# Performance work log

Measured on AMD Instinct MI355X. Metric: run time of the kernel, lower is better.

## Reference

```python
import jax, jax.numpy as jnp
import numpy as np

BN_EPS = 1e-5

# Octonion multiplication table: hamilton block (r, c) = SIGN[c][r] * a[IDX[c][r]]
IDX = np.array([
    [0,1,2,3,4,5,6,7],
    [1,0,3,2,5,4,7,6],
    [2,3,0,1,6,7,4,5],
    [3,2,1,0,7,6,5,4],
    [4,5,6,7,0,1,2,3],
    [5,4,7,6,1,0,3,2],
    [6,7,4,5,2,3,0,1],
    [7,6,5,4,3,2,1,0]], dtype=np.int32)
SIGN = np.array([
    [ 1, 1, 1, 1, 1, 1, 1, 1],
    [ 1,-1, 1,-1, 1,-1,-1, 1],
    [ 1,-1,-1, 1, 1, 1,-1,-1],
    [ 1, 1,-1,-1, 1,-1, 1,-1],
    [ 1,-1,-1,-1,-1, 1, 1, 1],
    [ 1, 1,-1, 1,-1,-1,-1, 1],
    [ 1, 1, 1,-1,-1, 1,-1,-1],
    [ 1,-1, 1, 1,-1,-1, 1,-1]], dtype=np.float32)

def make_octonion_mul(kernel):
    # kernel: [in/8, out]; split cols into 8 chunks a0..a7 of [in/8, out/8]
    in8, out = kernel.shape
    out8 = out // 8
    a = kernel.reshape(in8, 8, out8).transpose(1, 0, 2)  # [8, in/8, out/8]
    blocks = jnp.asarray(SIGN)[:, :, None, None] * a[jnp.asarray(IDX)]  # [c, r, in/8, out/8]
    # hamilton[r*in8:(r+1)*in8, c*out8:(c+1)*out8] = blocks[c, r]
    return jnp.transpose(blocks, (1, 2, 0, 3)).reshape(8 * in8, out)  # [in, out]

def setup_inputs() -> dict:
    key = jax.random.key(0)
    ks = jax.random.split(key, 5)
    N, E, D_IN, D_OUT = 100000, 3200000, 256, 256
    stdv = float(np.sqrt(6.0 / (D_IN // 8 + D_OUT)))
    return {
        "x": jax.random.normal(ks[0], (N, D_IN), dtype=jnp.float32),
        "weight": jax.random.uniform(ks[1], (D_IN // 8, D_OUT), dtype=jnp.float32,
                                      minval=-stdv, maxval=stdv),
        "gamma": jnp.ones((D_OUT,), dtype=jnp.float32),
        "beta": jnp.zeros((D_OUT,), dtype=jnp.float32),
        "edge_weight": jax.random.uniform(ks[2], (E,), dtype=jnp.float32),
        "edge_src": jax.random.randint(ks[3], (E,), 0, N, dtype=jnp.int32),
        "edge_dst": jax.random.randint(ks[4], (E,), 0, N, dtype=jnp.int32),
    }

def reference(x, weight, gamma, beta, edge_weight, edge_src, edge_dst):
    N = x.shape[0]
    hamilton = make_octonion_mul(weight)          # [in, out]
    support = x @ hamilton                        # [N, out]
    # sparse adjacency aggregation: out[dst] += w * support[src]
    msgs = edge_weight[:, None] * support[edge_src]
    out = jax.ops.segment_sum(msgs, edge_dst, num_segments=N)  # [N, out]
    # BatchNorm1d (training mode: batch stats, biased variance)
    mean = jnp.mean(out, axis=0)
    var = jnp.var(out, axis=0)
    out = (out - mean) * jax.lax.rsqrt(var + BN_EPS) * gamma + beta
    return jnp.tanh(out)
```

## Files before the change

kernel.cpp:

```cpp
#include <hip/hip_runtime.h>
#include <cmath>

#define NB 1024
#define CHUNK 16384

typedef short short8 __attribute__((ext_vector_type(8)));
typedef float f32x4 __attribute__((ext_vector_type(4)));

__constant__ int c_IDX[64] = {
  0,1,2,3,4,5,6,7,
  1,0,3,2,5,4,7,6,
  2,3,0,1,6,7,4,5,
  3,2,1,0,7,6,5,4,
  4,5,6,7,0,1,2,3,
  5,4,7,6,1,0,3,2,
  6,7,4,5,2,3,0,1,
  7,6,5,4,3,2,1,0};
__constant__ float c_SIGN[64] = {
  1,1,1,1,1,1,1,1,
  1,-1,1,-1,1,-1,-1,1,
  1,-1,-1,1,1,1,-1,-1,
  1,1,-1,-1,1,-1,1,-1,
  1,-1,-1,-1,-1,1,1,1,
  1,1,-1,1,-1,-1,-1,1,
  1,1,1,-1,-1,1,-1,-1,
  1,-1,1,1,-1,-1,1,-1};

__device__ inline unsigned bf16_rne(float f) {
  unsigned u = __float_as_uint(f);
  return (u + 0x7fffu + ((u >> 16) & 1u)) >> 16;
}
__device__ inline unsigned bfpack(float lo, float hi) {
  return bf16_rne(lo) | (bf16_rne(hi) << 16);
}

__global__ __launch_bounds__(256) void hamT_kernel(const float* __restrict__ weight,
                                                   unsigned short* __restrict__ hi,
                                                   unsigned short* __restrict__ lo,
                                                   int* __restrict__ binTot,
                                                   float* __restrict__ bnsum) {
  if (blockIdx.x == 0) {
    #pragma unroll
    for (int k = 0; k < NB / 256; k++) binTot[k * 256 + threadIdx.x] = 0;
    bnsum[threadIdx.x] = 0.f;
    bnsum[256 + threadIdx.x] = 0.f;
  }
  int idx = blockIdx.x * 256 + threadIdx.x;
  int col = idx >> 8, k = idx & 255;
  int r = k >> 5, i = k & 31, c = col >> 5, o = col & 31;
  float v = c_SIGN[c * 8 + r] * weight[i * 256 + c_IDX[c * 8 + r] * 32 + o];
  unsigned hb = bf16_rne(v);
  float hf = __uint_as_float(hb << 16);
  hi[idx] = (unsigned short)hb;
  lo[idx] = (unsigned short)bf16_rne(v - hf);
}

__global__ __launch_bounds__(256) void cvt_kernel(const float4* __restrict__ x4,
                                                  uint2* __restrict__ xh, size_t n4) {
  size_t idx = (size_t)blockIdx.x * 256 + threadIdx.x;
  size_t stride = (size_t)gridDim.x * 256;
  for (size_t i = idx; i < n4; i += stride) {
    float4 v = x4[i];
    xh[i] = make_uint2(bfpack(v.x, v.y), bfpack(v.z, v.w));
  }
}

__global__ __launch_bounds__(256) void binhist_kernel(const int* __restrict__ dst,
                                                      int* __restrict__ binTot,
                                                      int E, int N) {
  __shared__ int h[NB];
  int tid = threadIdx.x;
  for (int i = tid; i < NB; i += 256) h[i] = 0;
  __syncthreads();
  int base = blockIdx.x * CHUNK;
  int end = base + CHUNK; if (end > E) end = E;
  for (int i = base + tid; i < end; i += 256)
    atomicAdd(&h[(int)((long long)dst[i] * NB / N)], 1);
  __syncthreads();
  for (int i = tid; i < NB; i += 256)
    if (h[i]) atomicAdd(&binTot[i], h[i]);
}

__global__ __launch_bounds__(1024) void binscan_kernel(const int* __restrict__ binTot,
                                                       int* __restrict__ binStart,
                                                       int* __restrict__ binCursor, int E) {
  __shared__ int wsum[16], wbase[16];
  int tid = threadIdx.x, lane = tid & 63, wid = tid >> 6;
  int v = binTot[tid];
  int incl = v;
  #pragma unroll
  for (int d = 1; d < 64; d <<= 1) { int u = __shfl_up(incl, d); if (lane >= d) incl += u; }
  if (lane == 63) wsum[wid] = incl;
  __syncthreads();
  if (tid == 0) { int s = 0; for (int w = 0; w < 16; w++) { wbase[w] = s; s += wsum[w]; } }
  __syncthreads();
  int excl = wbase[wid] + incl - v;
  binStart[tid] = excl;
  binCursor[tid] = excl;
  if (tid == NB - 1) binStart[NB] = E;
}

__global__ __launch_bounds__(256) void bin_scatter(const int* __restrict__ src,
                                                   const int* __restrict__ dst,
                                                   const float* __restrict__ w,
                                                   int* __restrict__ binCursor,
                                                   int2* __restrict__ bb, int E, int N) {
  __shared__ int hist[NB];
  __shared__ int lcur[NB];
  int tid = threadIdx.x;
  int base = blockIdx.x * CHUNK;
  int end = base + CHUNK; if (end > E) end = E;
  for (int i = tid; i < NB; i += 256) hist[i] = 0;
  __syncthreads();
  for (int i = base + tid; i < end; i += 256)
    atomicAdd(&hist[(int)((long long)dst[i] * NB / N)], 1);
  __syncthreads();
  for (int i = tid; i < NB; i += 256) {
    int h = hist[i];
    lcur[i] = h ? atomicAdd(&binCursor[i], h) : 0;
  }
  __syncthreads();
  for (int i = base + tid; i < end; i += 256) {
    int d = dst[i];
    int b = (int)((long long)d * NB / N);
    int d0 = (int)(((long long)b * N + NB - 1) / NB);
    int pos = atomicAdd(&lcur[b], 1);
    bb[pos] = make_int2(src[i] | ((d - d0) << 24), __float_as_int(w[i]));
  }
}

__global__ __launch_bounds__(256) void bin_place(const int2* __restrict__ bb,
                                                 const int* __restrict__ binStart,
                                                 int* __restrict__ off,
                                                 int* __restrict__ cnt,
                                                 int2* __restrict__ edges, int N) {
  __shared__ int lcnt[104];
  __shared__ int loff[104];
  int b = blockIdx.x, tid = threadIdx.x;
  int d0 = (int)(((long long)b * N + NB - 1) / NB);
  int d1 = (int)(((long long)(b + 1) * N + NB - 1) / NB);
  if (d1 > N) d1 = N;
  int nd = d1 - d0;
  int e0 = binStart[b], e1 = binStart[b + 1];
  for (int i = tid; i < nd; i += 256) lcnt[i] = 0;
  __syncthreads();
  for (int i = e0 + tid; i < e1; i += 256)
    atomicAdd(&lcnt[((unsigned)bb[i].x) >> 24], 1);
  __syncthreads();
  if (tid == 0) {
    int s = e0;
    for (int i = 0; i < nd; i++) { loff[i] = s; s += lcnt[i]; }
  }
  __syncthreads();
  for (int i = tid; i < nd; i += 256) {
    off[d0 + i] = loff[i];
    cnt[d0 + i] = lcnt[i];
  }
  __syncthreads();
  for (int i = tid; i < nd; i += 256) lcnt[i] = loff[i];
  __syncthreads();
  for (int i = e0 + tid; i < e1; i += 256) {
    int2 e = bb[i];
    int pos = atomicAdd(&lcnt[((unsigned)e.x) >> 24], 1);
    edges[pos] = make_int2(e.x & 0xFFFFFF, e.y);
  }
}

__device__ inline void acc4(float& a0, float& a1, float& a2, float& a3,
                            uint2 v, float w) {
  a0 = fmaf(w, __uint_as_float(v.x << 16), a0);
  a1 = fmaf(w, __uint_as_float(v.x & 0xffff0000u), a1);
  a2 = fmaf(w, __uint_as_float(v.y << 16), a2);
  a3 = fmaf(w, __uint_as_float(v.y & 0xffff0000u), a3);
}

__global__ __launch_bounds__(256) void gather_kernel(const uint2* __restrict__ x8,
                                                     const int2* __restrict__ edges,
                                                     const int* __restrict__ off,
                                                     const int* __restrict__ cnt,
                                                     uint2* __restrict__ agg8, int N) {
  int d = blockIdx.x * 4 + (threadIdx.x >> 6);
  if (d >= N) return;
  int c = threadIdx.x & 63;
  int start = off[d], n = cnt[d];
  float a0 = 0.f, a1 = 0.f, a2 = 0.f, a3 = 0.f;
  int t = 0;
  for (; t + 8 <= n; t += 8) {
    int2 e0 = edges[start + t + 0];
    int2 e1 = edges[start + t + 1];
    int2 e2 = edges[start + t + 2];
    int2 e3 = edges[start + t + 3];
    int2 e4 = edges[start + t + 4];
    int2 e5 = edges[start + t + 5];
    int2 e6 = edges[start + t + 6];
    int2 e7 = edges[start + t + 7];
    uint2 v0 = x8[(size_t)e0.x * 64 + c];
    uint2 v1 = x8[(size_t)e1.x * 64 + c];
    uint2 v2 = x8[(size_t)e2.x * 64 + c];
    uint2 v3 = x8[(size_t)e3.x * 64 + c];
    uint2 v4 = x8[(size_t)e4.x * 64 + c];
    uint2 v5 = x8[(size_t)e5.x * 64 + c];
    uint2 v6 = x8[(size_t)e6.x * 64 + c];
    uint2 v7 = x8[(size_t)e7.x * 64 + c];
    acc4(a0, a1, a2, a3, v0, __int_as_float(e0.y));
    acc4(a0, a1, a2, a3, v1, __int_as_float(e1.y));
    acc4(a0, a1, a2, a3, v2, __int_as_float(e2.y));
    acc4(a0, a1, a2, a3, v3, __int_as_float(e3.y));
    acc4(a0, a1, a2, a3, v4, __int_as_float(e4.y));
    acc4(a0, a1, a2, a3, v5, __int_as_float(e5.y));
    acc4(a0, a1, a2, a3, v6, __int_as_float(e6.y));
    acc4(a0, a1, a2, a3, v7, __int_as_float(e7.y));
  }
  for (; t < n; t++) {
    int2 e0 = edges[start + t];
    uint2 v0 = x8[(size_t)e0.x * 64 + c];
    acc4(a0, a1, a2, a3, v0, __int_as_float(e0.y));
  }
  agg8[(size_t)d * 64 + c] = make_uint2(bfpack(a0, a1), bfpack(a2, a3));
}

__global__ __launch_bounds__(512) void mfma_gemm(const uint4* __restrict__ aggh,
                                                 const unsigned short* __restrict__ hamT_hi,
                                                 const unsigned short* __restrict__ hamT_lo,
                                                 float* __restrict__ bnsum,
                                                 float* __restrict__ out, int N) {
  __shared__ __align__(16) unsigned short Al[128 * 256];
  __shared__ float csum[256], csq[256];
  const int tid = threadIdx.x;
  const int row0 = blockIdx.x * 128;
  const int lane = tid & 63, wv = tid >> 6;
  const int wm = wv >> 2, wn = wv & 3;

  if (tid < 256) { csum[tid] = 0.f; csq[tid] = 0.f; }

  #pragma unroll
  for (int it = 0; it < 8; it++) {
    int cidx = it * 512 + tid;
    int row = cidx >> 5, c16 = cidx & 31;
    int rg = row0 + row;
    uint4 v = make_uint4(0u, 0u, 0u, 0u);
    if (rg < N) v = aggh[(size_t)rg * 32 + c16];
    *(uint4*)((char*)Al + row * 512 + ((c16 * 16) ^ ((row & 7) << 4))) = v;
  }
  __syncthreads();

  f32x4 acc[4][4];
  #pragma unroll
  for (int m = 0; m < 4; m++)
    #pragma unroll
    for (int n = 0; n < 4; n++) acc[m][n] = (f32x4)0.f;

  const char* bh = (const char*)hamT_hi;
  const char* bl = (const char*)hamT_lo;
  #pragma unroll
  for (int kk = 0; kk < 8; kk++) {
    const int kbyte = (lane >> 4) * 16 + kk * 64;
    short8 af[4];
    #pragma unroll
    for (int m = 0; m < 4; m++) {
      int row = wm * 64 + m * 16 + (lane & 15);
      af[m] = *(const short8*)((const char*)Al + row * 512 + (kbyte ^ ((row & 7) << 4)));
    }
    #pragma unroll
    for (int n = 0; n < 4; n++) {
      int colg = wn * 64 + n * 16 + (lane & 15);
      size_t boff = (size_t)colg * 512 + kbyte;
      short8 bhv = *(const short8*)(bh + boff);
      short8 blv = *(const short8*)(bl + boff);
      #pragma unroll
      for (int m = 0; m < 4; m++)
        acc[m][n] = __builtin_amdgcn_mfma_f32_16x16x32_bf16(af[m], bhv, acc[m][n], 0, 0, 0);
      #pragma unroll
      for (int m = 0; m < 4; m++)
        acc[m][n] = __builtin_amdgcn_mfma_f32_16x16x32_bf16(af[m], blv, acc[m][n], 0, 0, 0);
    }
  }

  #pragma unroll
  for (int n = 0; n < 4; n++) {
    int colg = wn * 64 + n * 16 + (lane & 15);
    float s = 0.f, q = 0.f;
    #pragma unroll
    for (int m = 0; m < 4; m++) {
      int rgb = row0 + wm * 64 + m * 16 + (lane >> 4) * 4;
      #pragma unroll
      for (int r = 0; r < 4; r++) {
        float v = acc[m][n][r];
        s += v; q = fmaf(v, v, q);
        int rg = rgb + r;
        if (rg < N) out[(size_t)rg * 256 + colg] = v;
      }
    }
    s += __shfl_xor(s, 16); s += __shfl_xor(s, 32);
    q += __shfl_xor(q, 16); q += __shfl_xor(q, 32);
    if (lane < 16) {
      atomicAdd(&csum[wn * 64 + n * 16 + lane], s);
      atomicAdd(&csq [wn * 64 + n * 16 + lane], q);
    }
  }
  __syncthreads();
  if (tid < 256) {
    atomicAdd(&bnsum[tid], csum[tid]);
    atomicAdd(&bnsum[256 + tid], csq[tid]);
  }
}

__global__ __launch_bounds__(256) void final_kernel(float* __restrict__ out,
                                                    const float* __restrict__ bnsum,
                                                    const float* __restrict__ gamma,
                                                    const float* __restrict__ beta,
                                                    float invN, size_t total4) {
  size_t idx = (size_t)blockIdx.x * 256 + threadIdx.x;
  size_t stride = (size_t)gridDim.x * 256;
  int c0 = (int)((idx * 4) & 255);
  float sc[4], ofs[4];
  #pragma unroll
  for (int j = 0; j < 4; j++) {
    float mean = bnsum[c0 + j] * invN;
    float var  = bnsum[256 + c0 + j] * invN - mean * mean;
    float s = rsqrtf(var + 1e-5f) * gamma[c0 + j];
    sc[j] = s;
    ofs[j] = beta[c0 + j] - mean * s;
  }
  float4* out4 = (float4*)out;
  for (size_t i = idx; i < total4; i += stride) {
    float4 v = out4[i];
    v.x = tanhf(fmaf(v.x, sc[0], ofs[0]));
    v.y = tanhf(fmaf(v.y, sc[1], ofs[1]));
    v.z = tanhf(fmaf(v.z, sc[2], ofs[2]));
    v.w = tanhf(fmaf(v.w, sc[3], ofs[3]));
    out4[i] = v;
  }
}

extern "C" void kernel_launch(void* const* d_in, const int* in_sizes, int n_in,
                              void* d_out, int out_size, void* d_ws, size_t ws_size,
                              hipStream_t stream) {
  const float* x      = (const float*)d_in[0];
  const float* weight = (const float*)d_in[1];
  const float* gamma  = (const float*)d_in[2];
  const float* beta   = (const float*)d_in[3];
  const float* ew     = (const float*)d_in[4];
  const int*   esrc   = (const int*)d_in[5];
  const int*   edst   = (const int*)d_in[6];
  const int N = in_sizes[0] / 256;
  const int E = in_sizes[4];
  float* out = (float*)d_out;

  char* p = (char*)d_ws;
  auto alloc = [&](size_t bytes) {
    char* q = p;
    p += (bytes + 255) & ~(size_t)255;
    return q;
  };
  unsigned short* hamT_hi = (unsigned short*)alloc(65536 * 2);
  unsigned short* hamT_lo = (unsigned short*)alloc(65536 * 2);
  int*   binTot    = (int*)alloc(NB * 4);
  int*   binStart  = (int*)alloc((NB + 1) * 4);
  int*   binCursor = (int*)alloc(NB * 4);
  int*   cnt       = (int*)alloc((size_t)N * 4);
  int*   off       = (int*)alloc((size_t)N * 4);
  int2*  bb        = (int2*)alloc((size_t)E * 8);
  int2*  edges     = (int2*)alloc((size_t)E * 8);
  uint2* xh        = (uint2*)alloc((size_t)N * 256 * 2);
  uint4* aggh      = (uint4*)alloc((size_t)N * 256 * 2);
  float* bnsum     = (float*)alloc(512 * 4);

  const int gridE = (E + CHUNK - 1) / CHUNK;
  const int rowBlocks = (N + 127) / 128;

  hamT_kernel<<<256, 256, 0, stream>>>(weight, hamT_hi, hamT_lo, binTot, bnsum);
  cvt_kernel<<<2048, 256, 0, stream>>>((const float4*)x, xh, (size_t)N * 64);
  binhist_kernel<<<gridE, 256, 0, stream>>>(edst, binTot, E, N);
  binscan_kernel<<<1, 1024, 0, stream>>>(binTot, binStart, binCursor, E);
  bin_scatter<<<gridE, 256, 0, stream>>>(esrc, edst, ew, binCursor, bb, E, N);
  bin_place<<<NB, 256, 0, stream>>>(bb, binStart, off, cnt, edges, N);
  gather_kernel<<<(N + 3) / 4, 256, 0, stream>>>((const uint2*)xh, edges, off, cnt,
                                                 (uint2*)aggh, N);
  mfma_gemm<<<rowBlocks, 512, 0, stream>>>(aggh, hamT_hi, hamT_lo, bnsum, out, N);
  final_kernel<<<2048, 256, 0, stream>>>(out, bnsum, gamma, beta, 1.f / (float)N,
                                         (size_t)N * 64);
}
```

Measured before the change: 528.8 us.

## Sort edges by source window within dst, halve bins, store GEMM output as bf16

bin_place now sub-sorts each destination's edges by source-node window (13 windows of 8192 nodes), with a parallel block scan replacing the serial one. The aim is better cache locality for the gather's reads of source rows. The bin count drops to 512 and the chunk size to 8192, so each bin covers about 196 destinations. The GEMM writes its pre-BN output as bf16 into the reused bb buffer instead of fp32, which cuts the write and re-read traffic in the final kernel but adds rounding error before normalization.

```diff
diff --git a/kernel.cpp b/kernel.cpp
--- a/kernel.cpp
+++ b/kernel.cpp
@@ -1,8 +1,9 @@
 #include <hip/hip_runtime.h>
 #include <cmath>
 
-#define NB 1024
-#define CHUNK 16384
+#define NB 512
+#define CHUNK 8192
+#define NW 13
 
 typedef short short8 __attribute__((ext_vector_type(8)));
 typedef float f32x4 __attribute__((ext_vector_type(4)));
@@ -81,10 +82,10 @@
     if (h[i]) atomicAdd(&binTot[i], h[i]);
 }
 
-__global__ __launch_bounds__(1024) void binscan_kernel(const int* __restrict__ binTot,
-                                                       int* __restrict__ binStart,
-                                                       int* __restrict__ binCursor, int E) {
-  __shared__ int wsum[16], wbase[16];
+__global__ __launch_bounds__(512) void binscan_kernel(const int* __restrict__ binTot,
+                                                      int* __restrict__ binStart,
+                                                      int* __restrict__ binCursor, int E) {
+  __shared__ int wsum[8], wbase[8];
   int tid = threadIdx.x, lane = tid & 63, wid = tid >> 6;
   int v = binTot[tid];
   int incl = v;
@@ -92,7 +93,7 @@
   for (int d = 1; d < 64; d <<= 1) { int u = __shfl_up(incl, d); if (lane >= d) incl += u; }
   if (lane == 63) wsum[wid] = incl;
   __syncthreads();
-  if (tid == 0) { int s = 0; for (int w = 0; w < 16; w++) { wbase[w] = s; s += wsum[w]; } }
+  if (tid == 0) { int s = 0; for (int w = 0; w < 8; w++) { wbase[w] = s; s += wsum[w]; } }
   __syncthreads();
   int excl = wbase[wid] + incl - v;
   binStart[tid] = excl;
@@ -134,35 +135,60 @@
                                                  int* __restrict__ off,
                                                  int* __restrict__ cnt,
                                                  int2* __restrict__ edges, int N) {
-  __shared__ int lcnt[104];
-  __shared__ int loff[104];
+  __shared__ int lcnt[2560];
+  __shared__ int lscan[2561];
+  __shared__ int part[256];
+  __shared__ int wsum2[4];
   int b = blockIdx.x, tid = threadIdx.x;
   int d0 = (int)(((long long)b * N + NB - 1) / NB);
   int d1 = (int)(((long long)(b + 1) * N + NB - 1) / NB);
   if (d1 > N) d1 = N;
   int nd = d1 - d0;
+  int nk = nd * NW;
   int e0 = binStart[b], e1 = binStart[b + 1];
-  for (int i = tid; i < nd; i += 256) lcnt[i] = 0;
-  __syncthreads();
-  for (int i = e0 + tid; i < e1; i += 256)
-    atomicAdd(&lcnt[((unsigned)bb[i].x) >> 24], 1);
-  __syncthreads();
-  if (tid == 0) {
-    int s = e0;
-    for (int i = 0; i < nd; i++) { loff[i] = s; s += lcnt[i]; }
-  }
+  for (int i = tid; i < nk; i += 256) lcnt[i] = 0;
+  __syncthreads();
+  for (int i = e0 + tid; i < e1; i += 256) {
+    int ex = bb[i].x;
+    int win = (ex & 0xFFFFFF) >> 13; if (win >= NW) win = NW - 1;
+    atomicAdd(&lcnt[((unsigned)ex >> 24) * NW + win], 1);
+  }
+  __syncthreads();
+  int K = (nk + 255) >> 8;
+  int s = 0;
+  for (int k = 0; k < K; k++) { int i = tid * K + k; if (i < nk) s += lcnt[i]; }
+  part[tid] = s;
+  __syncthreads();
+  {
+    int lane = tid & 63, wid = tid >> 6;
+    int v = part[tid];
+    int incl = v;
+    #pragma unroll
+    for (int d = 1; d < 64; d <<= 1) { int u = __shfl_up(incl, d); if (lane >= d) incl += u; }
+    if (lane == 63) wsum2[wid] = incl;
+    __syncthreads();
+    if (tid == 0) { int t2 = 0; for (int w2 = 0; w2 < 4; w2++) { int tmp = wsum2[w2]; wsum2[w2] = t2; t2 += tmp; } }
+    __syncthreads();
+    s = wsum2[wid] + incl - v;
+  }
+  for (int k = 0; k < K; k++) {
+    int i = tid * K + k;
+    if (i < nk) { lscan[i] = s; s += lcnt[i]; }
+  }
+  __syncthreads();
+  if (tid == 0) lscan[nk] = e1 - e0;
   __syncthreads();
   for (int i = tid; i < nd; i += 256) {
-    off[d0 + i] = loff[i];
-    cnt[d0 + i] = lcnt[i];
-  }
-  __syncthreads();
-  for (int i = tid; i < nd; i += 256) lcnt[i] = loff[i];
+    off[d0 + i] = e0 + lscan[i * NW];
+    cnt[d0 + i] = lscan[(i + 1) * NW] - lscan[i * NW];
+  }
+  for (int i = tid; i < nk; i += 256) lcnt[i] = lscan[i];
   __syncthreads();
   for (int i = e0 + tid; i < e1; i += 256) {
     int2 e = bb[i];
-    int pos = atomicAdd(&lcnt[((unsigned)e.x) >> 24], 1);
-    edges[pos] = make_int2(e.x & 0xFFFFFF, e.y);
+    int win = (e.x & 0xFFFFFF) >> 13; if (win >= NW) win = NW - 1;
+    int pos = atomicAdd(&lcnt[((unsigned)e.x >> 24) * NW + win], 1);
+    edges[e0 + pos] = make_int2(e.x & 0xFFFFFF, e.y);
   }
 }
 
@@ -223,7 +249,7 @@
                                                  const unsigned short* __restrict__ hamT_hi,
                                                  const unsigned short* __restrict__ hamT_lo,
                                                  float* __restrict__ bnsum,
-                                                 float* __restrict__ out, int N) {
+                                                 unsigned short* __restrict__ obuf, int N) {
   __shared__ __align__(16) unsigned short Al[128 * 256];
   __shared__ float csum[256], csq[256];
   const int tid = threadIdx.x;
@@ -288,7 +314,7 @@
         float v = acc[m][n][r];
         s += v; q = fmaf(v, v, q);
         int rg = rgb + r;
-        if (rg < N) out[(size_t)rg * 256 + colg] = v;
+        if (rg < N) obuf[(size_t)rg * 256 + colg] = (unsigned short)bf16_rne(v);
       }
     }
     s += __shfl_xor(s, 16); s += __shfl_xor(s, 32);
@@ -305,7 +331,8 @@
   }
 }
 
-__global__ __launch_bounds__(256) void final_kernel(float* __restrict__ out,
+__global__ __launch_bounds__(256) void final_kernel(const uint2* __restrict__ obuf,
+                                                    float* __restrict__ out,
                                                     const float* __restrict__ bnsum,
                                                     const float* __restrict__ gamma,
                                                     const float* __restrict__ beta,
@@ -324,11 +351,12 @@
   }
   float4* out4 = (float4*)out;
   for (size_t i = idx; i < total4; i += stride) {
-    float4 v = out4[i];
-    v.x = tanhf(fmaf(v.x, sc[0], ofs[0]));
-    v.y = tanhf(fmaf(v.y, sc[1], ofs[1]));
-    v.z = tanhf(fmaf(v.z, sc[2], ofs[2]));
-    v.w = tanhf(fmaf(v.w, sc[3], ofs[3]));
+    uint2 u = obuf[i];
+    float4 v;
+    v.x = tanhf(fmaf(__uint_as_float(u.x << 16),         sc[0], ofs[0]));
+    v.y = tanhf(fmaf(__uint_as_float(u.x & 0xffff0000u), sc[1], ofs[1]));
+    v.z = tanhf(fmaf(__uint_as_float(u.y << 16),         sc[2], ofs[2]));
+    v.w = tanhf(fmaf(__uint_as_float(u.y & 0xffff0000u), sc[3], ofs[3]));
     out4[i] = v;
   }
 }
@@ -365,6 +393,7 @@
   uint2* xh        = (uint2*)alloc((size_t)N * 256 * 2);
   uint4* aggh      = (uint4*)alloc((size_t)N * 256 * 2);
   float* bnsum     = (float*)alloc(512 * 4);
+  unsigned short* obuf = (unsigned short*)bb;
 
   const int gridE = (E + CHUNK - 1) / CHUNK;
   const int rowBlocks = (N + 127) / 128;
@@ -372,12 +401,12 @@
   hamT_kernel<<<256, 256, 0, stream>>>(weight, hamT_hi, hamT_lo, binTot, bnsum);
   cvt_kernel<<<2048, 256, 0, stream>>>((const float4*)x, xh, (size_t)N * 64);
   binhist_kernel<<<gridE, 256, 0, stream>>>(edst, binTot, E, N);
-  binscan_kernel<<<1, 1024, 0, stream>>>(binTot, binStart, binCursor, E);
+  binscan_kernel<<<1, 512, 0, stream>>>(binTot, binStart, binCursor, E);
   bin_scatter<<<gridE, 256, 0, stream>>>(esrc, edst, ew, binCursor, bb, E, N);
   bin_place<<<NB, 256, 0, stream>>>(bb, binStart, off, cnt, edges, N);
   gather_kernel<<<(N + 3) / 4, 256, 0, stream>>>((const uint2*)xh, edges, off, cnt,
                                                  (uint2*)aggh, N);
-  mfma_gemm<<<rowBlocks, 512, 0, stream>>>(aggh, hamT_hi, hamT_lo, bnsum, out, N);
-  final_kernel<<<2048, 256, 0, stream>>>(out, bnsum, gamma, beta, 1.f / (float)N,
-                                         (size_t)N * 64);
-}
+  mfma_gemm<<<rowBlocks, 512, 0, stream>>>(aggh, hamT_hi, hamT_lo, bnsum, obuf, N);
+  final_kernel<<<2048, 256, 0, stream>>>((const uint2*)obuf, out, bnsum, gamma, beta,
+                                         1.f / (float)N, (size_t)N * 64);
+}
```

After: 515.0 us. -2.6%, faster.
